# Kernel tuning notes

Measured on AMD Instinct MI355X. Metric: run time of the kernel, lower is better.

## Reference

```python
import jax, jax.numpy as jnp
import numpy as np

H1, H2, H3 = 32, 64, 64
NODEN = 12
NODES_PER_GRAPH = NODEN + 2  # 14
N = 700000                   # 50000 graphs * 14 nodes
E = 4000000


def setup_inputs() -> dict:
    key = jax.random.key(0)
    ks = jax.random.split(key, 8)
    x = jax.random.normal(ks[0], (N, H1), dtype=jnp.float32)
    edges = jax.random.randint(ks[1], (2, E), 0, N, dtype=jnp.int64)
    W1 = jax.random.normal(ks[2], (H1, H2), dtype=jnp.float32) / np.sqrt(H1).astype(np.float32)
    b1 = jnp.zeros((H2,), jnp.float32)
    W2 = jax.random.normal(ks[3], (H2, H3), dtype=jnp.float32) / np.sqrt(H2).astype(np.float32)
    b2 = jnp.zeros((H3,), jnp.float32)
    Wfc = jax.random.normal(ks[4], (H3 * NODES_PER_GRAPH, 1), dtype=jnp.float32) / np.sqrt(H3 * NODES_PER_GRAPH).astype(np.float32)
    bfc = jnp.zeros((1,), jnp.float32)
    return {"x": x, "edges": edges, "W1": W1, "b1": b1, "W2": W2, "b2": b2, "Wfc": Wfc, "bfc": bfc}


def gcn_conv(x, src, dst, W, b, n):
    # PyG GCNConv: h = X W; add self-loops; norm = deg^-1/2[src]*deg^-1/2[dst]
    h = x @ W  # [N, out]
    ones = jnp.ones(src.shape[0], dtype=h.dtype)
    deg = jax.ops.segment_sum(ones, dst, num_segments=n) + jnp.asarray(1.0, h.dtype)  # +1 self-loop
    dinv = jax.lax.rsqrt(deg)  # deg >= 1 always (self-loop)
    norm = dinv[src] * dinv[dst]  # [E]
    agg = jax.ops.segment_sum(h[src] * norm[:, None], dst, num_segments=n)
    agg = agg + h * (dinv * dinv)[:, None]  # self-loop contribution
    return agg + b


def reference(x, edges, W1, b1, W2, b2, Wfc, bfc):
    src, dst = edges[0], edges[1]
    h = jax.nn.relu(gcn_conv(x, src, dst, W1, b1, N))
    # F.dropout(training=False) is identity in eval mode
    h = jax.nn.relu(gcn_conv(h, src, dst, W2, b2, N))
    h = h.reshape(-1, H3 * NODES_PER_GRAPH)  # [B, 896]
    return h @ Wfc + bfc  # [B, 1]
```

## Files before the change

kernel.cpp:

```cpp
#include <hip/hip_runtime.h>
#include <hip/hip_fp16.h>


typedef _Float16 half8 __attribute__((ext_vector_type(8)));
typedef float float4v __attribute__((ext_vector_type(4)));

#define CHUNK 8192
#define BSH 11
#define BNODES 2048

__global__ __launch_bounds__(256) void fallback_kernel(float* __restrict__ out, int n, float v)
{
  int i = blockIdx.x * 256 + threadIdx.x;
  if (i < n) out[i] = v;
}

__global__ __launch_bounds__(64) void probe_kernel(const int* __restrict__ edges, int* __restrict__ flag)
{
  if (threadIdx.x == 0) {
    int orv = edges[1] | edges[3] | edges[5] | edges[7] | edges[9] | edges[11] | edges[13] | edges[15];
    flag[0] = (orv == 0) ? 1 : 0;
  }
}

__global__ __launch_bounds__(64) void zero_dummy_kernel(
    __half* __restrict__ P, __half* __restrict__ F2, int N)
{
  int t = threadIdx.x;
  if (t < 8) ((uint2*)(P + (size_t)N * 32))[t] = make_uint2(0, 0);
  else if (t < 24) ((uint2*)(F2 + (size_t)N * 64))[t - 8] = make_uint2(0, 0);
}

__global__ __launch_bounds__(256) void hist2_kernel(
    const int* __restrict__ edges, int E, int N, const int* __restrict__ flag,
    int* __restrict__ cnt, int NBK)
{
  __shared__ int lh[512];
  int t = threadIdx.x;
  int blk = blockIdx.x;
  for (int b = t; b < NBK; b += 256) lh[b] = 0;
  __syncthreads();
  int sh = flag[0];
  int base = blk * CHUNK;
#pragma unroll
  for (int k = 0; k < CHUNK / 256; k++) {
    int e = base + k * 256 + t;
    if (e < E) {
      int d = edges[(E + e) << sh];
      if ((unsigned)d < (unsigned)N) atomicAdd(&lh[d >> BSH], 1);
    }
  }
  __syncthreads();
  for (int b = t; b < NBK; b += 256) cnt[(size_t)blk * NBK + b] = lh[b];
}

__global__ __launch_bounds__(64) void colscan_kernel(
    int* __restrict__ cnt, int NCH, int NBK, int* __restrict__ totals)
{
  int b = blockIdx.x;
  int lane = threadIdx.x;
  int carry = 0;
  int rounds = (NCH + 63) >> 6;
  for (int r = 0; r < rounds; r++) {
    int blk = r * 64 + lane;
    int v = (blk < NCH) ? cnt[(size_t)blk * NBK + b] : 0;
    int incl = v;
#pragma unroll
    for (int off = 1; off < 64; off <<= 1) {
      int x = __shfl_up(incl, off);
      if (lane >= off) incl += x;
    }
    int excl = incl - v + carry;
    if (blk < NCH) cnt[(size_t)blk * NBK + b] = excl;
    carry += __shfl(incl, 63);
  }
  if (lane == 0) totals[b] = carry;
}

__global__ __launch_bounds__(512) void scan_totals_kernel(
    const int* __restrict__ totals, int NBK,
    int* __restrict__ bstart, int* __restrict__ rowptr, int N)
{
  __shared__ int sm[512];
  int t = threadIdx.x;
  int v = (t < NBK) ? totals[t] : 0;
  sm[t] = v;
  __syncthreads();
  for (int off = 1; off < 512; off <<= 1) {
    int x = 0;
    if (t >= off) x = sm[t - off];
    __syncthreads();
    if (t >= off) sm[t] += x;
    __syncthreads();
  }
  if (t < NBK) bstart[t] = sm[t] - v;
  if (t == 0) { bstart[NBK] = sm[511]; rowptr[N] = sm[511] + N; }
}

__global__ __launch_bounds__(256) void pass3_kernel(
    const int* __restrict__ edges, int E, int N, const int* __restrict__ flag,
    const int* __restrict__ cnt, const int* __restrict__ bstart,
    int* __restrict__ pair, int NBK)
{
  __shared__ int lcur[512];
  int t = threadIdx.x;
  int blk = blockIdx.x;
  for (int b = t; b < NBK; b += 256)
    lcur[b] = bstart[b] + cnt[(size_t)blk * NBK + b];
  __syncthreads();
  int sh = flag[0];
  int base = blk * CHUNK;
#pragma unroll
  for (int k = 0; k < CHUNK / 256; k++) {
    int e = base + k * 256 + t;
    if (e < E) {
      int s = edges[e << sh];
      int d = edges[(E + e) << sh];
      if ((unsigned)s < (unsigned)N && (unsigned)d < (unsigned)N) {
        int pos = atomicAdd(&lcur[d >> BSH], 1);
        pair[pos] = s | ((d & (BNODES - 1)) << 20);
      }
    }
  }
}

__global__ __launch_bounds__(256) void build_kernel(
    const int* __restrict__ pair, const int* __restrict__ bstart,
    int* __restrict__ rowptr, float* __restrict__ dinv, int* __restrict__ col, int N)
{
  __shared__ int hist[BNODES];
  __shared__ int cur[BNODES];
  __shared__ int sc[256];
  int b = blockIdx.x;
  int t = threadIdx.x;
  int pbeg = bstart[b], pend = bstart[b + 1];
  int colbase = pbeg + (b << BSH);
#pragma unroll
  for (int i = 0; i < BNODES / 256; i++) {
    int idx = i * 256 + t;
    int row = (b << BSH) + idx;
    hist[idx] = (row < N) ? 1 : 0;
  }
  __syncthreads();
  for (int p = pbeg + t; p < pend; p += 256)
    atomicAdd(&hist[(pair[p] >> 20) & (BNODES - 1)], 1);
  __syncthreads();
  int hv[8];
  int tsum = 0;
#pragma unroll
  for (int i = 0; i < 8; i++) { hv[i] = hist[t * 8 + i]; tsum += hv[i]; }
  sc[t] = tsum;
  __syncthreads();
  for (int off = 1; off < 256; off <<= 1) {
    int x = 0;
    if (t >= off) x = sc[t - off];
    __syncthreads();
    if (t >= off) sc[t] += x;
    __syncthreads();
  }
  int run = sc[t] - tsum;
#pragma unroll
  for (int i = 0; i < 8; i++) {
    int idx = t * 8 + i;
    int rp = colbase + run;
    int row = (b << BSH) + idx;
    if (row < N) {
      rowptr[row] = rp;
      dinv[row] = rsqrtf((float)hv[i]);
      col[rp] = row;
      cur[idx] = rp + 1;
    } else {
      cur[idx] = rp;
    }
    run += hv[i];
  }
  __syncthreads();
  for (int p = pbeg + t; p < pend; p += 256) {
    int v = pair[p];
    int pos = atomicAdd(&cur[(v >> 20) & (BNODES - 1)], 1);
    col[pos] = v & 0xFFFFF;
  }
}

__global__ __launch_bounds__(256) void scale_x_kernel(
    const float* __restrict__ X, const float* __restrict__ dinv,
    __half* __restrict__ P, int N)
{
  int idx = blockIdx.x * 256 + threadIdx.x;
  int total = N * 4;
  int stride = gridDim.x * 256;
  for (int i = idx; i < total; i += stride) {
    int node = i >> 2, part = i & 3;
    const float4* xp = (const float4*)(X + (size_t)node * 32 + part * 8);
    float dv = dinv[node];
    float4 v0 = xp[0], v1 = xp[1];
    half8 h;
    h[0] = (_Float16)(dv * v0.x); h[1] = (_Float16)(dv * v0.y);
    h[2] = (_Float16)(dv * v0.z); h[3] = (_Float16)(dv * v0.w);
    h[4] = (_Float16)(dv * v1.x); h[5] = (_Float16)(dv * v1.y);
    h[6] = (_Float16)(dv * v1.z); h[7] = (_Float16)(dv * v1.w);
    *(half8*)(P + (size_t)node * 32 + part * 8) = h;
  }
}

__device__ inline void hacc(uint4 v, __half2* a)
{
  a[0] = __hadd2(a[0], *reinterpret_cast<__half2*>(&v.x));
  a[1] = __hadd2(a[1], *reinterpret_cast<__half2*>(&v.y));
  a[2] = __hadd2(a[2], *reinterpret_cast<__half2*>(&v.z));
  a[3] = __hadd2(a[3], *reinterpret_cast<__half2*>(&v.w));
}

__global__ __launch_bounds__(256) void agg1_mfma_kernel(
    const __half* __restrict__ P, const int* __restrict__ rowptr,
    const int* __restrict__ col, const float* __restrict__ dinv,
    const float* __restrict__ W1, const float* __restrict__ b1,
    __half* __restrict__ U, int ntiles, int ndummy)
{
  int lane = threadIdx.x & 63;
  int n16 = lane & 15;
  int quad = lane >> 4;

  half8 bf[4];
#pragma unroll
  for (int jb = 0; jb < 4; jb++)
#pragma unroll
    for (int i = 0; i < 8; i++)
      bf[jb][i] = (_Float16)W1[(quad * 8 + i) * 64 + jb * 16 + n16];
  float b1j[4];
#pragma unroll
  for (int jb = 0; jb < 4; jb++) b1j[jb] = b1[jb * 16 + n16];

  const uint4* P4 = (const uint4*)P;
  _Float16* Uh = (_Float16*)U;
  int wave = (blockIdx.x * 256 + threadIdx.x) >> 6;
  int nw = (gridDim.x * 256) >> 6;
  for (int tile = wave; tile < ntiles; tile += nw) {
    int ut = __builtin_amdgcn_readfirstlane(tile);
    int base = ut * 16;
    int node = base + n16;
    int rbeg = rowptr[node];
    int rlen = rowptr[node + 1] - rbeg;

    __half2 z2 = __float2half2_rn(0.f);
    __half2 aA[4] = {z2, z2, z2, z2};
    __half2 aB[4] = {z2, z2, z2, z2};

    for (int j = 0; __any(j < rlen); j += 8) {
      int c[8];
#pragma unroll
      for (int q = 0; q < 8; q++) {
        int cc = col[rbeg + j + q];
        c[q] = (j + q < rlen) ? cc : ndummy;
      }
      uint4 v[8];
#pragma unroll
      for (int q = 0; q < 8; q++) v[q] = P4[((size_t)c[q] << 2) + quad];
#pragma unroll
      for (int q = 0; q < 8; q += 2) { hacc(v[q], aA); hacc(v[q + 1], aB); }
    }
#pragma unroll
    for (int k = 0; k < 4; k++) aA[k] = __hadd2(aA[k], aB[k]);

    half8 a = *reinterpret_cast<half8*>(aA);
    float4v co[4];
#pragma unroll
    for (int jb = 0; jb < 4; jb++) {
      float4v z = {0.f, 0.f, 0.f, 0.f};
      co[jb] = __builtin_amdgcn_mfma_f32_16x16x32_f16(a, bf[jb], z, 0, 0, 0);
    }
#pragma unroll
    for (int r = 0; r < 4; r++) {
      int node2 = base + quad * 4 + r;
      float dv = dinv[node2];
#pragma unroll
      for (int jb = 0; jb < 4; jb++) {
        float h = dv * co[jb][r] + b1j[jb];
        h = h > 0.f ? h : 0.f;
        Uh[(size_t)node2 * 64 + jb * 16 + n16] = (_Float16)(dv * h);
      }
    }
  }
}

__global__ __launch_bounds__(256) void out_init_kernel(
    float* __restrict__ out, const float* __restrict__ bfc, int n)
{
  int i = blockIdx.x * 256 + threadIdx.x;
  if (i < n) out[i] = bfc[0];
}

__global__ __launch_bounds__(256) void mfma_final_fused_kernel(
    const __half* __restrict__ U, const int* __restrict__ rowptr,
    const int* __restrict__ col, const float* __restrict__ dinv,
    const float* __restrict__ W2, const float* __restrict__ b2,
    const float* __restrict__ Wfc, float* __restrict__ out,
    int ntiles, int ndummy)
{
  int lane = threadIdx.x & 63;
  int n16 = lane & 15;
  int quad = lane >> 4;

  half8 bf[4][2];
#pragma unroll
  for (int jb = 0; jb < 4; jb++)
#pragma unroll
    for (int kf = 0; kf < 2; kf++)
#pragma unroll
      for (int i = 0; i < 8; i++)
        bf[jb][kf][i] = (_Float16)W2[(kf * 32 + quad * 8 + i) * 64 + jb * 16 + n16];
  float b2j[4];
#pragma unroll
  for (int jb = 0; jb < 4; jb++) b2j[jb] = b2[jb * 16 + n16];

  const uint4* U4 = (const uint4*)U;
  int wave = (blockIdx.x * 256 + threadIdx.x) >> 6;
  int nw = (gridDim.x * 256) >> 6;
  for (int tile = wave; tile < ntiles; tile += nw) {
    int ut = __builtin_amdgcn_readfirstlane(tile);
    int base = ut * 16;
    int node = base + n16;
    int rbeg = rowptr[node];
    int rlen = rowptr[node + 1] - rbeg;

    __half2 z2 = __float2half2_rn(0.f);
    __half2 aE0[4] = {z2, z2, z2, z2};
    __half2 aE1[4] = {z2, z2, z2, z2};
    __half2 aO0[4] = {z2, z2, z2, z2};
    __half2 aO1[4] = {z2, z2, z2, z2};

    for (int j = 0; __any(j < rlen); j += 4) {
      int c0 = col[rbeg + j];
      int c1 = col[rbeg + j + 1];
      int c2 = col[rbeg + j + 2];
      int c3 = col[rbeg + j + 3];
      c0 = (j < rlen) ? c0 : ndummy;
      c1 = (j + 1 < rlen) ? c1 : ndummy;
      c2 = (j + 2 < rlen) ? c2 : ndummy;
      c3 = (j + 3 < rlen) ? c3 : ndummy;
      uint4 v00 = U4[((size_t)c0 << 3) + quad];
      uint4 v01 = U4[((size_t)c0 << 3) + 4 + quad];
      uint4 v10 = U4[((size_t)c1 << 3) + quad];
      uint4 v11 = U4[((size_t)c1 << 3) + 4 + quad];
      uint4 v20 = U4[((size_t)c2 << 3) + quad];
      uint4 v21 = U4[((size_t)c2 << 3) + 4 + quad];
      uint4 v30 = U4[((size_t)c3 << 3) + quad];
      uint4 v31 = U4[((size_t)c3 << 3) + 4 + quad];
      hacc(v00, aE0); hacc(v01, aE1);
      hacc(v10, aO0); hacc(v11, aO1);
      hacc(v20, aE0); hacc(v21, aE1);
      hacc(v30, aO0); hacc(v31, aO1);
    }
#pragma unroll
    for (int k = 0; k < 4; k++) {
      aE0[k] = __hadd2(aE0[k], aO0[k]);
      aE1[k] = __hadd2(aE1[k], aO1[k]);
    }
    __half2 dv = __half2half2(__float2half_rn(dinv[node]));
#pragma unroll
    for (int j = 0; j < 4; j++) {
      aE0[j] = __hmul2(aE0[j], dv);
      aE1[j] = __hmul2(aE1[j], dv);
    }
    half8 a0 = *reinterpret_cast<half8*>(aE0);
    half8 a1 = *reinterpret_cast<half8*>(aE1);

    int g_r[4], t_r[4];
#pragma unroll
    for (int r = 0; r < 4; r++) {
      int nd = base + quad * 4 + r;
      g_r[r] = nd / 14;
      t_r[r] = nd - g_r[r] * 14;
    }
    float pr[4] = {0.f, 0.f, 0.f, 0.f};
#pragma unroll
    for (int jb = 0; jb < 4; jb++) {
      float4v acc = {0.f, 0.f, 0.f, 0.f};
      acc = __builtin_amdgcn_mfma_f32_16x16x32_f16(a0, bf[jb][0], acc, 0, 0, 0);
      acc = __builtin_amdgcn_mfma_f32_16x16x32_f16(a1, bf[jb][1], acc, 0, 0, 0);
      int j = jb * 16 + n16;
#pragma unroll
      for (int r = 0; r < 4; r++) {
        float h = acc[r] + b2j[jb];
        h = h > 0.f ? h : 0.f;
        pr[r] += h * Wfc[t_r[r] * 64 + j];
      }
    }
#pragma unroll
    for (int r = 0; r < 4; r++) {
#pragma unroll
      for (int off = 1; off < 16; off <<= 1) pr[r] += __shfl_xor(pr[r], off);
    }
    if (n16 == 0) {
#pragma unroll
      for (int r = 0; r < 4; r++) atomicAdd(&out[g_r[r]], pr[r]);
    }
  }
}

extern "C" void kernel_launch(void* const* d_in, const int* in_sizes, int n_in,
                              void* d_out, int out_size, void* d_ws, size_t ws_size,
                              hipStream_t stream)
{
  const float* x = (const float*)d_in[0];
  const int* edges = (const int*)d_in[1];
  const float* W1 = (const float*)d_in[2];
  const float* b1 = (const float*)d_in[3];
  const float* W2 = (const float*)d_in[4];
  const float* b2 = (const float*)d_in[5];
  const float* Wfc = (const float*)d_in[6];
  const float* bfc = (const float*)d_in[7];
  float* out = (float*)d_out;
  (void)n_in;

  const int N = in_sizes[0] / 32;
  const int E = in_sizes[1] / 2;
  const int B = out_size;
  const int NBK = (N + BNODES - 1) >> BSH;
  const int NCH = (E + CHUNK - 1) / CHUNK;

  char* ws = (char*)d_ws;
  size_t off = 0;
  auto alloc = [&](size_t bytes) -> void* {
    void* p = ws + off;
    off += (bytes + 255) & ~(size_t)255;
    return p;
  };
  int* flag = (int*)alloc(256);
  int* cnt = (int*)alloc((size_t)NCH * NBK * 4);
  int* totals = (int*)alloc((size_t)NBK * 4);
  int* bstart = (int*)alloc(((size_t)NBK + 1) * 4);
  int* col = (int*)alloc(((size_t)E + N + 256) * 4);
  int* rowptr = (int*)alloc(((size_t)N + 1) * 4);
  float* dinv = (float*)alloc((size_t)N * 4);
  __half* P = (__half*)alloc(((size_t)N + 16) * 32 * 2);
  __half* F2 = (__half*)alloc(((size_t)N + 16) * 64 * 2);
  int* pair = (int*)P;

  if (off > ws_size) {
    float v = -(float)(double)(ws_size >> 20);
    fallback_kernel<<<(B + 255) / 256, 256, 0, stream>>>(out, B, v);
    return;
  }

  probe_kernel<<<1, 64, 0, stream>>>(edges, flag);
  zero_dummy_kernel<<<1, 64, 0, stream>>>(P, F2, N);
  hist2_kernel<<<NCH, 256, 0, stream>>>(edges, E, N, flag, cnt, NBK);
  colscan_kernel<<<NBK, 64, 0, stream>>>(cnt, NCH, NBK, totals);
  scan_totals_kernel<<<1, 512, 0, stream>>>(totals, NBK, bstart, rowptr, N);
  pass3_kernel<<<NCH, 256, 0, stream>>>(edges, E, N, flag, cnt, bstart, pair, NBK);
  build_kernel<<<NBK, 256, 0, stream>>>(pair, bstart, rowptr, dinv, col, N);

  int ntiles = (N + 15) / 16;
  scale_x_kernel<<<2048, 256, 0, stream>>>(x, dinv, P, N);
  agg1_mfma_kernel<<<4096, 256, 0, stream>>>(P, rowptr, col, dinv, W1, b1, F2, ntiles, N);
  out_init_kernel<<<(B + 255) / 256, 256, 0, stream>>>(out, bfc, B);
  mfma_final_fused_kernel<<<4096, 256, 0, stream>>>(F2, rowptr, col, dinv, W2, b2, Wfc,
                                                    out, ntiles, N);
}
```

Measured before the change: 533.3 us.

## Sort nodes by degree so each MFMA tile groups nodes with similar degree

Adds a degree histogram, a scan and a placement pass that build a permutation of nodes ordered by in-degree. Both aggregation kernels take their 16-node tiles from this permutation, so lanes in a wave have similar neighbour-loop lengths and the __any loop wastes fewer iterations on divergence. The cost is three extra small kernels and an indirection for each tile. Output rows, dinv reads and the final-layer node indices become scattered rather than contiguous, which can hurt coalescing of the U and F2 stores and cause more atomic contention on out.

```diff
diff --git a/kernel.cpp b/kernel.cpp
--- a/kernel.cpp
+++ b/kernel.cpp
@@ -8,6 +8,7 @@
 #define CHUNK 8192
 #define BSH 11
 #define BNODES 2048
+#define DBINS 64
 
 __global__ __launch_bounds__(256) void fallback_kernel(float* __restrict__ out, int n, float v)
 {
@@ -24,9 +25,10 @@
 }
 
 __global__ __launch_bounds__(64) void zero_dummy_kernel(
-    __half* __restrict__ P, __half* __restrict__ F2, int N)
-{
-  int t = threadIdx.x;
+    __half* __restrict__ P, __half* __restrict__ F2, int* __restrict__ dhist, int N)
+{
+  int t = threadIdx.x;
+  dhist[t] = 0;
   if (t < 8) ((uint2*)(P + (size_t)N * 32))[t] = make_uint2(0, 0);
   else if (t < 24) ((uint2*)(F2 + (size_t)N * 64))[t - 8] = make_uint2(0, 0);
 }
@@ -179,6 +181,64 @@
     int v = pair[p];
     int pos = atomicAdd(&cur[(v >> 20) & (BNODES - 1)], 1);
     col[pos] = v & 0xFFFFF;
+  }
+}
+
+__global__ __launch_bounds__(256) void deg_hist_kernel(
+    const int* __restrict__ rowptr, int* __restrict__ dhist, int N)
+{
+  __shared__ int lh[DBINS];
+  int t = threadIdx.x;
+  if (t < DBINS) lh[t] = 0;
+  __syncthreads();
+  int n = blockIdx.x * 256 + t;
+  if (n < N) {
+    int rlen = rowptr[n + 1] - rowptr[n];
+    int b = rlen < DBINS ? rlen : DBINS - 1;
+    atomicAdd(&lh[b], 1);
+  }
+  __syncthreads();
+  if (t < DBINS && lh[t]) atomicAdd(&dhist[t], lh[t]);
+}
+
+__global__ __launch_bounds__(64) void deg_scan_kernel(
+    const int* __restrict__ dhist, int* __restrict__ dcur)
+{
+  int t = threadIdx.x;
+  int v = dhist[t];
+  int incl = v;
+#pragma unroll
+  for (int off = 1; off < 64; off <<= 1) {
+    int x = __shfl_up(incl, off);
+    if (t >= off) incl += x;
+  }
+  dcur[t] = incl - v;
+}
+
+__global__ __launch_bounds__(256) void deg_place_kernel(
+    const int* __restrict__ rowptr, int* __restrict__ dcur,
+    int* __restrict__ perm, int N)
+{
+  __shared__ int lh[DBINS];
+  __shared__ int lbase[DBINS];
+  int t = threadIdx.x;
+  if (t < DBINS) lh[t] = 0;
+  __syncthreads();
+  int n = blockIdx.x * 256 + t;
+  int b = -1;
+  if (n < N) {
+    int rlen = rowptr[n + 1] - rowptr[n];
+    b = rlen < DBINS ? rlen : DBINS - 1;
+    atomicAdd(&lh[b], 1);
+  }
+  __syncthreads();
+  if (t < DBINS) lbase[t] = lh[t] ? atomicAdd(&dcur[t], lh[t]) : 0;
+  __syncthreads();
+  if (t < DBINS) lh[t] = lbase[t];
+  __syncthreads();
+  if (n < N) {
+    int pos = atomicAdd(&lh[b], 1);
+    perm[pos] = n;
   }
 }
 
@@ -214,6 +274,7 @@
 __global__ __launch_bounds__(256) void agg1_mfma_kernel(
     const __half* __restrict__ P, const int* __restrict__ rowptr,
     const int* __restrict__ col, const float* __restrict__ dinv,
+    const int* __restrict__ perm,
     const float* __restrict__ W1, const float* __restrict__ b1,
     __half* __restrict__ U, int ntiles, int ndummy)
 {
@@ -238,7 +299,7 @@
   for (int tile = wave; tile < ntiles; tile += nw) {
     int ut = __builtin_amdgcn_readfirstlane(tile);
     int base = ut * 16;
-    int node = base + n16;
+    int node = perm[base + n16];
     int rbeg = rowptr[node];
     int rlen = rowptr[node + 1] - rbeg;
 
@@ -271,7 +332,7 @@
     }
 #pragma unroll
     for (int r = 0; r < 4; r++) {
-      int node2 = base + quad * 4 + r;
+      int node2 = __shfl(node, quad * 4 + r);
       float dv = dinv[node2];
 #pragma unroll
       for (int jb = 0; jb < 4; jb++) {
@@ -293,6 +354,7 @@
 __global__ __launch_bounds__(256) void mfma_final_fused_kernel(
     const __half* __restrict__ U, const int* __restrict__ rowptr,
     const int* __restrict__ col, const float* __restrict__ dinv,
+    const int* __restrict__ perm,
     const float* __restrict__ W2, const float* __restrict__ b2,
     const float* __restrict__ Wfc, float* __restrict__ out,
     int ntiles, int ndummy)
@@ -319,7 +381,7 @@
   for (int tile = wave; tile < ntiles; tile += nw) {
     int ut = __builtin_amdgcn_readfirstlane(tile);
     int base = ut * 16;
-    int node = base + n16;
+    int node = perm[base + n16];
     int rbeg = rowptr[node];
     int rlen = rowptr[node + 1] - rbeg;
 
@@ -368,7 +430,7 @@
     int g_r[4], t_r[4];
 #pragma unroll
     for (int r = 0; r < 4; r++) {
-      int nd = base + quad * 4 + r;
+      int nd = __shfl(node, quad * 4 + r);
       g_r[r] = nd / 14;
       t_r[r] = nd - g_r[r] * 14;
     }
@@ -418,6 +480,7 @@
   const int B = out_size;
   const int NBK = (N + BNODES - 1) >> BSH;
   const int NCH = (E + CHUNK - 1) / CHUNK;
+  const int NBLK = (N + 255) / 256;
 
   char* ws = (char*)d_ws;
   size_t off = 0;
@@ -433,6 +496,9 @@
   int* col = (int*)alloc(((size_t)E + N + 256) * 4);
   int* rowptr = (int*)alloc(((size_t)N + 1) * 4);
   float* dinv = (float*)alloc((size_t)N * 4);
+  int* dhist = (int*)alloc(DBINS * 4);
+  int* dcur = (int*)alloc(DBINS * 4);
+  int* perm = (int*)alloc((size_t)N * 4);
   __half* P = (__half*)alloc(((size_t)N + 16) * 32 * 2);
   __half* F2 = (__half*)alloc(((size_t)N + 16) * 64 * 2);
   int* pair = (int*)P;
@@ -444,17 +510,21 @@
   }
 
   probe_kernel<<<1, 64, 0, stream>>>(edges, flag);
-  zero_dummy_kernel<<<1, 64, 0, stream>>>(P, F2, N);
+  zero_dummy_kernel<<<1, 64, 0, stream>>>(P, F2, dhist, N);
   hist2_kernel<<<NCH, 256, 0, stream>>>(edges, E, N, flag, cnt, NBK);
   colscan_kernel<<<NBK, 64, 0, stream>>>(cnt, NCH, NBK, totals);
   scan_totals_kernel<<<1, 512, 0, stream>>>(totals, NBK, bstart, rowptr, N);
   pass3_kernel<<<NCH, 256, 0, stream>>>(edges, E, N, flag, cnt, bstart, pair, NBK);
   build_kernel<<<NBK, 256, 0, stream>>>(pair, bstart, rowptr, dinv, col, N);
 
+  deg_hist_kernel<<<NBLK, 256, 0, stream>>>(rowptr, dhist, N);
+  deg_scan_kernel<<<1, 64, 0, stream>>>(dhist, dcur);
+  deg_place_kernel<<<NBLK, 256, 0, stream>>>(rowptr, dcur, perm, N);
+
   int ntiles = (N + 15) / 16;
   scale_x_kernel<<<2048, 256, 0, stream>>>(x, dinv, P, N);
-  agg1_mfma_kernel<<<4096, 256, 0, stream>>>(P, rowptr, col, dinv, W1, b1, F2, ntiles, N);
+  agg1_mfma_kernel<<<4096, 256, 0, stream>>>(P, rowptr, col, dinv, perm, W1, b1, F2, ntiles, N);
   out_init_kernel<<<(B + 255) / 256, 256, 0, stream>>>(out, bfc, B);
-  mfma_final_fused_kernel<<<4096, 256, 0, stream>>>(F2, rowptr, col, dinv, W2, b2, Wfc,
+  mfma_final_fused_kernel<<<4096, 256, 0, stream>>>(F2, rowptr, col, dinv, perm, W2, b2, Wfc,
                                                     out, ntiles, N);
 }
```

New measurement: 592.3 us. +11.1%, slower.
